# Optimization experiments

Hardware: AMD Instinct MI355X
Metric: run time of the kernel (lower is better)

Reference implementation:

```python
import jax, jax.numpy as jnp
import numpy as np

ALPHA = 100.0
EPS = 1e-12  # matches torch F.normalize default eps


def l2norm(v, axis):
    n = jnp.linalg.norm(v, axis=axis, keepdims=True)
    return v / jnp.maximum(n, EPS)


def setup_inputs() -> dict:
    key = jax.random.key(0)
    k1, k2 = jax.random.split(key)
    x = jax.random.normal(k1, (32, 128, 64, 64), dtype=jnp.float32)
    centroids = jax.random.uniform(k2, (64, 128), dtype=jnp.float32)
    return {"x": x, "centroids": centroids}


def reference(x, centroids):
    N, C, H, W = x.shape
    K = centroids.shape[0]
    # descriptor-wise L2 normalization over channel dim
    x = l2norm(x, axis=1)
    xf = x.reshape(N, C, H * W)  # [N, C, S]
    # 1x1 conv with weight = 2*alpha*centroids, bias = -alpha*||centroids||
    bias = -ALPHA * jnp.linalg.norm(centroids, axis=1)  # [K]
    logits = 2.0 * ALPHA * jnp.einsum('kc,ncs->nks', centroids, xf) + bias[None, :, None]
    a = jax.nn.softmax(logits, axis=1)  # soft assignment over clusters, [N, K, S]
    # vlad[n,k,c] = sum_s a[n,k,s] * (x[n,c,s] - centroids[k,c])
    #            = (a @ x^T)       - (sum_s a) * centroids   (GEMM form)
    vlad = jnp.einsum('nks,ncs->nkc', a, xf) - a.sum(axis=-1)[:, :, None] * centroids[None, :, :]
    vlad = l2norm(vlad, axis=2)            # intra-normalization
    vlad = vlad.reshape(N, K * C)
    vlad = l2norm(vlad, axis=1)            # final L2 normalization
    return vlad
```

## Files before the change

kernel.cpp:

```cpp
#include <hip/hip_runtime.h>
#include <math.h>

#define ALPHA_F 100.0f

constexpr int N_ = 32, C_ = 128, K_ = 64, S_ = 4096;
constexpr int NCHUNK = 8, SCHUNK = S_ / NCHUNK;
constexpr int ST = 128, NSUB = SCHUNK / ST;
constexpr int NT = 512;

typedef __attribute__((ext_vector_type(8))) short bf16x8;
typedef __attribute__((ext_vector_type(4))) float f32x4;

__device__ __forceinline__ short f2b(float f) {
  union { float f; unsigned u; } v; v.f = f;
  unsigned r = v.u + 0x7FFFu + ((v.u >> 16) & 1u);
  return (short)(r >> 16);
}
__device__ __forceinline__ float b2f(short b) {
  union { unsigned u; float f; } v; v.u = ((unsigned)(unsigned short)b) << 16;
  return v.f;
}
__device__ __forceinline__ unsigned pk2(short a, short b) {
  return ((unsigned)(unsigned short)a) | (((unsigned)(unsigned short)b) << 16);
}
#define BARRIER() do { asm volatile("s_waitcnt lgkmcnt(0)" ::: "memory"); \
                       __builtin_amdgcn_s_barrier(); } while (0)

__global__ __launch_bounds__(NT, 2)
void nv_stage1(const float* __restrict__ x, const float* __restrict__ cent,
               float* __restrict__ vlad_part, float* __restrict__ asum_part) {
  __shared__ short x2h[ST][136];
  __shared__ short x2l[ST][136];
  __shared__ short xbh[C_][136];
  __shared__ short cl_s[K_][136];
  __shared__ short a_th[K_][136];
  __shared__ float invn_s[ST];
  __shared__ float bias_s[K_];

  float* scratch = (float*)&a_th[0][0];

  const int t = threadIdx.x;
  const int l = t & 63, w = t >> 6;
  const int l16 = l & 15, g = l >> 4;
  const int cq = t >> 4, so = t & 15;
  const int chunk = blockIdx.x, n = blockIdx.y;
  const int sb = w * 16, cb = w * 16;

  const float* xg = x + (size_t)n * C_ * S_ + (size_t)chunk * SCHUNK;

  float xr[4][8];
  #pragma unroll
  for (int i = 0; i < 4; ++i) {
    const float* p = xg + (size_t)(cq * 4 + i) * S_ + so * 8;
    float4 u = *(const float4*)p, v = *(const float4*)(p + 4);
    xr[i][0] = u.x; xr[i][1] = u.y; xr[i][2] = u.z; xr[i][3] = u.w;
    xr[i][4] = v.x; xr[i][5] = v.y; xr[i][6] = v.z; xr[i][7] = v.w;
  }

  {
    const float* cr = cent + (t & 63) * C_ + w * 16;
    float ss = 0.f;
    #pragma unroll
    for (int h = 0; h < 4; ++h) {
      float4 v = *(const float4*)(cr + h * 4);
      ss += v.x * v.x + v.y * v.y + v.z * v.z + v.w * v.w;
    }
    scratch[w * 64 + (t & 63)] = ss;
  }
  {
    const int k = t >> 3, c0 = (t & 7) * 16;
    const float* cr = cent + k * C_ + c0;
    unsigned* dst = (unsigned*)&cl_s[k][c0];
    #pragma unroll
    for (int h = 0; h < 4; ++h) {
      float4 v = *(const float4*)(cr + h * 4);
      short a0 = f2b(v.x - b2f(f2b(v.x))), a1 = f2b(v.y - b2f(f2b(v.y)));
      short a2 = f2b(v.z - b2f(f2b(v.z))), a3 = f2b(v.w - b2f(f2b(v.w)));
      dst[h * 2 + 0] = pk2(a0, a1);
      dst[h * 2 + 1] = pk2(a2, a3);
    }
  }
  bf16x8 chf[4][4];
  #pragma unroll
  for (int nt2 = 0; nt2 < 4; ++nt2)
    #pragma unroll
    for (int ks = 0; ks < 4; ++ks) {
      const float* cr = cent + (nt2 * 16 + l16) * C_ + ks * 32 + g * 8;
      float4 a = *(const float4*)cr, b = *(const float4*)(cr + 4);
      bf16x8 f;
      f[0] = f2b(a.x); f[1] = f2b(a.y); f[2] = f2b(a.z); f[3] = f2b(a.w);
      f[4] = f2b(b.x); f[5] = f2b(b.y); f[6] = f2b(b.z); f[7] = f2b(b.w);
      chf[nt2][ks] = f;
    }
  __syncthreads();
  if (t < 64) {
    float ss = 0.f;
    #pragma unroll
    for (int q = 0; q < 8; ++q) ss += scratch[q * 64 + t];
    bias_s[t] = -ALPHA_F * sqrtf(ss);
  }
  __syncthreads();
  float bias_r[4];
  #pragma unroll
  for (int nt2 = 0; nt2 < 4; ++nt2) bias_r[nt2] = bias_s[nt2 * 16 + l16];

  f32x4 acc2[4];
  #pragma unroll
  for (int nt2 = 0; nt2 < 4; ++nt2) { f32x4 z = {0.f, 0.f, 0.f, 0.f}; acc2[nt2] = z; }
  float asum_acc[4] = {0.f, 0.f, 0.f, 0.f};

  for (int st = 0; st < NSUB; ++st) {
    BARRIER();
    float ss[8];
    #pragma unroll
    for (int j = 0; j < 8; ++j)
      ss[j] = xr[0][j] * xr[0][j] + xr[1][j] * xr[1][j]
            + xr[2][j] * xr[2][j] + xr[3][j] * xr[3][j];
    #pragma unroll
    for (int j = 0; j < 8; ++j) {
      ss[j] += __shfl_xor(ss[j], 16);
      ss[j] += __shfl_xor(ss[j], 32);
    }
    if (g == 0) {
      float4 w0 = make_float4(ss[0], ss[1], ss[2], ss[3]);
      float4 w1 = make_float4(ss[4], ss[5], ss[6], ss[7]);
      *(float4*)&scratch[w * 132 + so * 8]     = w0;
      *(float4*)&scratch[w * 132 + so * 8 + 4] = w1;
    }
    BARRIER();
    if (t < ST) {
      float s2 = 0.f;
      #pragma unroll
      for (int q = 0; q < 8; ++q) s2 += scratch[q * 132 + t];
      invn_s[t] = 1.0f / fmaxf(sqrtf(s2), 1e-12f);
    }
    BARRIER();
    {
      float4 i0 = *(float4*)&invn_s[so * 8], i1 = *(float4*)&invn_s[so * 8 + 4];
      float inj[8] = {i0.x, i0.y, i0.z, i0.w, i1.x, i1.y, i1.z, i1.w};
      #pragma unroll
      for (int i = 0; i < 4; ++i)
        #pragma unroll
        for (int j = 0; j < 8; ++j) xr[i][j] *= inj[j];
      #pragma unroll
      for (int i = 0; i < 4; ++i) {
        bf16x8 r;
        #pragma unroll
        for (int j = 0; j < 8; ++j) r[j] = f2b(xr[i][j]);
        *(bf16x8*)&xbh[cq * 4 + i][so * 8] = r;
      }
      #pragma unroll
      for (int j = 0; j < 8; ++j) {
        int s = so * 8 + j;
        int pc = (((cq >> 1) ^ (so & 7)) * 8) + (cq & 1) * 4;
        short h0 = f2b(xr[0][j]), h1 = f2b(xr[1][j]);
        short h2 = f2b(xr[2][j]), h3 = f2b(xr[3][j]);
        uint2 ph; ph.x = pk2(h0, h1); ph.y = pk2(h2, h3);
        *(uint2*)&x2h[s][pc] = ph;
        short e0 = f2b(xr[0][j] - b2f(h0)), e1 = f2b(xr[1][j] - b2f(h1));
        short e2 = f2b(xr[2][j] - b2f(h2)), e3 = f2b(xr[3][j] - b2f(h3));
        uint2 pl; pl.x = pk2(e0, e1); pl.y = pk2(e2, e3);
        *(uint2*)&x2l[s][pc] = pl;
      }
    }
    if (st + 1 < NSUB) {
      const float* pg = xg + (st + 1) * ST + so * 8;
      #pragma unroll
      for (int i = 0; i < 4; ++i) {
        const float* p = pg + (size_t)(cq * 4 + i) * S_;
        float4 u = *(const float4*)p, v = *(const float4*)(p + 4);
        xr[i][0] = u.x; xr[i][1] = u.y; xr[i][2] = u.z; xr[i][3] = u.w;
        xr[i][4] = v.x; xr[i][5] = v.y; xr[i][6] = v.z; xr[i][7] = v.w;
      }
    }
    BARRIER();
    bf16x8 ah[4], al[4];
    {
      int s = sb + l16;
      int nu = (s >> 3) & 7;
      #pragma unroll
      for (int ks = 0; ks < 4; ++ks) {
        int pc = ((ks * 4 + g) ^ nu) * 8;
        ah[ks] = *(const bf16x8*)&x2h[s][pc];
        al[ks] = *(const bf16x8*)&x2l[s][pc];
      }
    }
    f32x4 acc1[4];
    #pragma unroll
    for (int nt2 = 0; nt2 < 4; ++nt2) { f32x4 z = {0.f, 0.f, 0.f, 0.f}; acc1[nt2] = z; }
    #pragma unroll
    for (int nt2 = 0; nt2 < 4; ++nt2)
      #pragma unroll
      for (int ks = 0; ks < 4; ++ks) {
        acc1[nt2] = __builtin_amdgcn_mfma_f32_16x16x32_bf16(ah[ks], chf[nt2][ks], acc1[nt2], 0, 0, 0);
        acc1[nt2] = __builtin_amdgcn_mfma_f32_16x16x32_bf16(al[ks], chf[nt2][ks], acc1[nt2], 0, 0, 0);
        bf16x8 clf = *(const bf16x8*)&cl_s[nt2 * 16 + l16][ks * 32 + g * 8];
        acc1[nt2] = __builtin_amdgcn_mfma_f32_16x16x32_bf16(ah[ks], clf, acc1[nt2], 0, 0, 0);
      }
    {
      float v[4][4];
      #pragma unroll
      for (int nt2 = 0; nt2 < 4; ++nt2)
        #pragma unroll
        for (int i = 0; i < 4; ++i)
          v[nt2][i] = 2.f * ALPHA_F * acc1[nt2][i] + bias_r[nt2];
      float mx[4], sm[4];
      #pragma unroll
      for (int i = 0; i < 4; ++i) {
        mx[i] = fmaxf(fmaxf(v[0][i], v[1][i]), fmaxf(v[2][i], v[3][i]));
        mx[i] = fmaxf(mx[i], __shfl_xor(mx[i], 1));
        mx[i] = fmaxf(mx[i], __shfl_xor(mx[i], 2));
        mx[i] = fmaxf(mx[i], __shfl_xor(mx[i], 4));
        mx[i] = fmaxf(mx[i], __shfl_xor(mx[i], 8));
        sm[i] = 0.f;
      }
      #pragma unroll
      for (int nt2 = 0; nt2 < 4; ++nt2)
        #pragma unroll
        for (int i = 0; i < 4; ++i) {
          float e = __expf(v[nt2][i] - mx[i]);
          v[nt2][i] = e; sm[i] += e;
        }
      #pragma unroll
      for (int i = 0; i < 4; ++i) {
        sm[i] += __shfl_xor(sm[i], 1);
        sm[i] += __shfl_xor(sm[i], 2);
        sm[i] += __shfl_xor(sm[i], 4);
        sm[i] += __shfl_xor(sm[i], 8);
        sm[i] = 1.0f / sm[i];
      }
      #pragma unroll
      for (int nt2 = 0; nt2 < 4; ++nt2) {
        float a0 = v[nt2][0] * sm[0], a1 = v[nt2][1] * sm[1];
        float a2 = v[nt2][2] * sm[2], a3 = v[nt2][3] * sm[3];
        asum_acc[nt2] += a0 + a1 + a2 + a3;
        uint2 pa; pa.x = pk2(f2b(a0), f2b(a1)); pa.y = pk2(f2b(a2), f2b(a3));
        *(uint2*)&a_th[nt2 * 16 + l16][sb + g * 4] = pa;
      }
    }
    BARRIER();
    bf16x8 xq[4];
    #pragma unroll
    for (int ks = 0; ks < 4; ++ks)
      xq[ks] = *(const bf16x8*)&xbh[cb + l16][ks * 32 + g * 8];
    #pragma unroll
    for (int nt2 = 0; nt2 < 4; ++nt2)
      #pragma unroll
      for (int ks = 0; ks < 4; ++ks) {
        bf16x8 bq = *(const bf16x8*)&a_th[nt2 * 16 + l16][ks * 32 + g * 8];
        acc2[nt2] = __builtin_amdgcn_mfma_f32_16x16x32_bf16(xq[ks], bq, acc2[nt2], 0, 0, 0);
      }
  }

  BARRIER();
  #pragma unroll
  for (int nt2 = 0; nt2 < 4; ++nt2) {
    float vv = asum_acc[nt2];
    vv += __shfl_xor(vv, 16);
    vv += __shfl_xor(vv, 32);
    if (g == 0) scratch[2048 + w * 64 + nt2 * 16 + l16] = vv;
  }
  const size_t base = (size_t)(n * NCHUNK + chunk) * (K_ * C_);
  #pragma unroll
  for (int nt2 = 0; nt2 < 4; ++nt2) {
    int k = nt2 * 16 + l16;
    float4 o = make_float4(acc2[nt2][0], acc2[nt2][1], acc2[nt2][2], acc2[nt2][3]);
    *(float4*)&vlad_part[base + (size_t)k * C_ + cb + g * 4] = o;
  }
  BARRIER();
  if (t < 64) {
    float sum2 = 0.f;
    #pragma unroll
    for (int q = 0; q < 8; ++q) sum2 += scratch[2048 + q * 64 + t];
    asum_part[(n * NCHUNK + chunk) * K_ + t] = sum2;
  }
}

__global__ __launch_bounds__(256, 1)
void nv_stage2(const float* __restrict__ vlad_part, const float* __restrict__ asum_part,
               const float* __restrict__ cent, float* __restrict__ out) {
  __shared__ float asum_s[K_];
  __shared__ float redw[4];
  const int t = threadIdx.x, n = blockIdx.x;

  if (t < K_) {
    float s = 0.f;
    for (int ch = 0; ch < NCHUNK; ++ch) s += asum_part[(n * NCHUNK + ch) * K_ + t];
    asum_s[t] = s;
  }
  __syncthreads();

  float4 vp[8];
  float scl[8];
  float tot = 0.f;
  #pragma unroll
  for (int r = 0; r < 8; ++r) {
    const int f = t + 256 * r;
    const int k = f >> 5, c = (f & 31) * 4;
    float4 acc = make_float4(0.f, 0.f, 0.f, 0.f);
    for (int ch = 0; ch < NCHUNK; ++ch) {
      float4 v = *(const float4*)&vlad_part[((size_t)(n * NCHUNK + ch) * K_ + k) * C_ + c];
      acc.x += v.x; acc.y += v.y; acc.z += v.z; acc.w += v.w;
    }
    const float as = asum_s[k];
    float4 cw = *(const float4*)&cent[k * C_ + c];
    acc.x -= as * cw.x; acc.y -= as * cw.y; acc.z -= as * cw.z; acc.w -= as * cw.w;
    float ssq = acc.x * acc.x + acc.y * acc.y + acc.z * acc.z + acc.w * acc.w;
    #pragma unroll
    for (int wd = 1; wd <= 16; wd <<= 1) ssq += __shfl_xor(ssq, wd);
    float sc = 1.0f / fmaxf(sqrtf(ssq), 1e-12f);
    vp[r] = acc; scl[r] = sc;
    tot += ssq * sc * sc * (1.0f / 32.0f);
  }
  #pragma unroll
  for (int wd = 1; wd <= 32; wd <<= 1) tot += __shfl_xor(tot, wd);
  if ((t & 63) == 0) redw[t >> 6] = tot;
  __syncthreads();
  const float total = redw[0] + redw[1] + redw[2] + redw[3];
  const float rfin = 1.0f / fmaxf(sqrtf(total), 1e-12f);

  #pragma unroll
  for (int r = 0; r < 8; ++r) {
    const int f = t + 256 * r;
    const int k = f >> 5, c = (f & 31) * 4;
    const float s = scl[r] * rfin;
    float4 o = make_float4(vp[r].x * s, vp[r].y * s, vp[r].z * s, vp[r].w * s);
    *(float4*)&out[(size_t)n * (K_ * C_) + k * C_ + c] = o;
  }
}

extern "C" void kernel_launch(void* const* d_in, const int* in_sizes, int n_in,
                              void* d_out, int out_size, void* d_ws, size_t ws_size,
                              hipStream_t stream) {
  const float* x    = (const float*)d_in[0];
  const float* cent = (const float*)d_in[1];
  float* out = (float*)d_out;

  float* vlad_part = (float*)d_ws;
  float* asum_part = vlad_part + (size_t)N_ * NCHUNK * K_ * C_;

  dim3 g1(NCHUNK, N_);
  nv_stage1<<<g1, NT, 0, stream>>>(x, cent, vlad_part, asum_part);
  nv_stage2<<<N_, 256, 0, stream>>>(vlad_part, asum_part, cent, out);
}
```

Measured before the change: 46.47 us.

## Switch to fp16 split MFMA, defer normalization, double chunks, split stage2

Replaces the bf16 hi/lo split GEMMs with fp16 hi/lo split MFMAs. The first GEMM now runs on raw x loaded straight from global memory, and the per-column inverse norm is applied to the logits and assignments afterwards, so the normalized x2h/x2l LDS tiles are gone. LDS is packed into one byte buffer with swizzled centroid tiles. NCHUNK goes from 8 to 16 and the occupancy hint from 2 to 4 blocks per CU, for more parallelism. Stage 2 is split into a wider per-(n,k-block) kernel plus a small final-scaling kernel, which adds an extra launch and more global traffic. fp16 range and precision risks apply because raw x is unnormalized and x is now read from global memory twice.

After: 65.42 us. +40.8%, slower.

```diff
diff --git a/kernel.cpp b/kernel.cpp
--- a/kernel.cpp
+++ b/kernel.cpp
@@ -4,40 +4,37 @@
 #define ALPHA_F 100.0f
 
 constexpr int N_ = 32, C_ = 128, K_ = 64, S_ = 4096;
-constexpr int NCHUNK = 8, SCHUNK = S_ / NCHUNK;
+constexpr int NCHUNK = 16, SCHUNK = S_ / NCHUNK;
 constexpr int ST = 128, NSUB = SCHUNK / ST;
 constexpr int NT = 512;
 
-typedef __attribute__((ext_vector_type(8))) short bf16x8;
+typedef _Float16 f16;
+typedef __attribute__((ext_vector_type(4))) _Float16 f16x4;
+typedef __attribute__((ext_vector_type(8))) _Float16 f16x8;
 typedef __attribute__((ext_vector_type(4))) float f32x4;
 
-__device__ __forceinline__ short f2b(float f) {
-  union { float f; unsigned u; } v; v.f = f;
-  unsigned r = v.u + 0x7FFFu + ((v.u >> 16) & 1u);
-  return (short)(r >> 16);
-}
-__device__ __forceinline__ float b2f(short b) {
-  union { unsigned u; float f; } v; v.u = ((unsigned)(unsigned short)b) << 16;
-  return v.f;
-}
-__device__ __forceinline__ unsigned pk2(short a, short b) {
-  return ((unsigned)(unsigned short)a) | (((unsigned)(unsigned short)b) << 16);
-}
+constexpr int XBH = 0;
+constexpr int ASB = 34816;
+constexpr int CLS = 52224;
+constexpr int CHS = 68608;
+constexpr int INV = 80896;
+constexpr int BIA = 81408;
+constexpr int LDS_SZ = 81664;
+
 #define BARRIER() do { asm volatile("s_waitcnt lgkmcnt(0)" ::: "memory"); \
                        __builtin_amdgcn_s_barrier(); } while (0)
 
-__global__ __launch_bounds__(NT, 2)
+__global__ __launch_bounds__(NT, 4)
 void nv_stage1(const float* __restrict__ x, const float* __restrict__ cent,
                float* __restrict__ vlad_part, float* __restrict__ asum_part) {
-  __shared__ short x2h[ST][136];
-  __shared__ short x2l[ST][136];
-  __shared__ short xbh[C_][136];
-  __shared__ short cl_s[K_][136];
-  __shared__ short a_th[K_][136];
-  __shared__ float invn_s[ST];
-  __shared__ float bias_s[K_];
-
-  float* scratch = (float*)&a_th[0][0];
+  __shared__ __align__(16) unsigned char lds[LDS_SZ];
+  ushort* xbh  = (ushort*)(lds + XBH);
+  ushort* a_s  = (ushort*)(lds + ASB);
+  float*  scr  = (float*)(lds + ASB);
+  ushort* cls  = (ushort*)(lds + CLS);
+  ushort* chs  = (ushort*)(lds + CHS);
+  float*  invn = (float*)(lds + INV);
+  float*  bias_s = (float*)(lds + BIA);
 
   const int t = threadIdx.x;
   const int l = t & 63, w = t >> 6;
@@ -58,45 +55,49 @@
   }
 
   {
-    const float* cr = cent + (t & 63) * C_ + w * 16;
+    const float* cr = cent + l * C_ + w * 16;
     float ss = 0.f;
     #pragma unroll
     for (int h = 0; h < 4; ++h) {
       float4 v = *(const float4*)(cr + h * 4);
       ss += v.x * v.x + v.y * v.y + v.z * v.z + v.w * v.w;
     }
-    scratch[w * 64 + (t & 63)] = ss;
+    scr[w * 64 + l] = ss;
   }
   {
-    const int k = t >> 3, c0 = (t & 7) * 16;
-    const float* cr = cent + k * C_ + c0;
-    unsigned* dst = (unsigned*)&cl_s[k][c0];
-    #pragma unroll
-    for (int h = 0; h < 4; ++h) {
-      float4 v = *(const float4*)(cr + h * 4);
-      short a0 = f2b(v.x - b2f(f2b(v.x))), a1 = f2b(v.y - b2f(f2b(v.y)));
-      short a2 = f2b(v.z - b2f(f2b(v.z))), a3 = f2b(v.w - b2f(f2b(v.w)));
-      dst[h * 2 + 0] = pk2(a0, a1);
-      dst[h * 2 + 1] = pk2(a2, a3);
-    }
-  }
-  bf16x8 chf[4][4];
-  #pragma unroll
-  for (int nt2 = 0; nt2 < 4; ++nt2)
-    #pragma unroll
-    for (int ks = 0; ks < 4; ++ks) {
-      const float* cr = cent + (nt2 * 16 + l16) * C_ + ks * 32 + g * 8;
-      float4 a = *(const float4*)cr, b = *(const float4*)(cr + 4);
-      bf16x8 f;
-      f[0] = f2b(a.x); f[1] = f2b(a.y); f[2] = f2b(a.z); f[3] = f2b(a.w);
-      f[4] = f2b(b.x); f[5] = f2b(b.y); f[6] = f2b(b.z); f[7] = f2b(b.w);
-      chf[nt2][ks] = f;
-    }
+    const int k = t >> 3, c7 = t & 7;
+    const float* cr = cent + k * C_ + c7 * 16;
+    f16x8 lo0, lo1;
+    #pragma unroll
+    for (int h = 0; h < 8; ++h) {
+      float v0 = cr[h], v1 = cr[8 + h];
+      lo0[h] = (f16)(v0 - (float)((f16)v0));
+      lo1[h] = (f16)(v1 - (float)((f16)v1));
+    }
+    *(f16x8*)&cls[k * 128 + ((2 * c7) ^ (k & 15)) * 8]     = lo0;
+    *(f16x8*)&cls[k * 128 + ((2 * c7 + 1) ^ (k & 15)) * 8] = lo1;
+  }
+  if (t < 384) {
+    const int kl = t >> 3, c7 = t & 7;
+    const float* cr = cent + (16 + kl) * C_ + c7 * 16;
+    f16x8 h0v, h1v;
+    #pragma unroll
+    for (int h = 0; h < 8; ++h) { h0v[h] = (f16)cr[h]; h1v[h] = (f16)cr[8 + h]; }
+    *(f16x8*)&chs[kl * 128 + ((2 * c7) ^ (kl & 15)) * 8]     = h0v;
+    *(f16x8*)&chs[kl * 128 + ((2 * c7 + 1) ^ (kl & 15)) * 8] = h1v;
+  }
+  f16x8 chf0[4];
+  #pragma unroll
+  for (int ks = 0; ks < 4; ++ks) {
+    const float* cr = cent + l16 * C_ + ks * 32 + g * 8;
+    #pragma unroll
+    for (int h = 0; h < 8; ++h) chf0[ks][h] = (f16)cr[h];
+  }
   __syncthreads();
   if (t < 64) {
     float ss = 0.f;
     #pragma unroll
-    for (int q = 0; q < 8; ++q) ss += scratch[q * 64 + t];
+    for (int q = 0; q < 8; ++q) ss += scr[q * 64 + t];
     bias_s[t] = -ALPHA_F * sqrtf(ss);
   }
   __syncthreads();
@@ -106,105 +107,80 @@
 
   f32x4 acc2[4];
   #pragma unroll
-  for (int nt2 = 0; nt2 < 4; ++nt2) { f32x4 z = {0.f, 0.f, 0.f, 0.f}; acc2[nt2] = z; }
+  for (int nt2 = 0; nt2 < 4; ++nt2) { f32x4 z = {0.f,0.f,0.f,0.f}; acc2[nt2] = z; }
   float asum_acc[4] = {0.f, 0.f, 0.f, 0.f};
 
   for (int st = 0; st < NSUB; ++st) {
-    BARRIER();
-    float ss[8];
-    #pragma unroll
-    for (int j = 0; j < 8; ++j)
-      ss[j] = xr[0][j] * xr[0][j] + xr[1][j] * xr[1][j]
-            + xr[2][j] * xr[2][j] + xr[3][j] * xr[3][j];
-    #pragma unroll
-    for (int j = 0; j < 8; ++j) {
-      ss[j] += __shfl_xor(ss[j], 16);
-      ss[j] += __shfl_xor(ss[j], 32);
-    }
-    if (g == 0) {
-      float4 w0 = make_float4(ss[0], ss[1], ss[2], ss[3]);
-      float4 w1 = make_float4(ss[4], ss[5], ss[6], ss[7]);
-      *(float4*)&scratch[w * 132 + so * 8]     = w0;
-      *(float4*)&scratch[w * 132 + so * 8 + 4] = w1;
+    {
+      float ssj[8];
+      #pragma unroll
+      for (int j = 0; j < 8; ++j) {
+        ssj[j] = xr[0][j]*xr[0][j] + xr[1][j]*xr[1][j] + xr[2][j]*xr[2][j] + xr[3][j]*xr[3][j];
+        ssj[j] += __shfl_xor(ssj[j], 16);
+        ssj[j] += __shfl_xor(ssj[j], 32);
+      }
+      if (g == 0) {
+        *(float4*)&scr[w * 128 + so * 8]     = make_float4(ssj[0], ssj[1], ssj[2], ssj[3]);
+        *(float4*)&scr[w * 128 + so * 8 + 4] = make_float4(ssj[4], ssj[5], ssj[6], ssj[7]);
+      }
+      #pragma unroll
+      for (int i = 0; i < 4; ++i) {
+        f16x8 r;
+        #pragma unroll
+        for (int j = 0; j < 8; ++j) r[j] = (f16)xr[i][j];
+        *(f16x8*)&xbh[(cq * 4 + i) * 136 + so * 8] = r;
+      }
     }
     BARRIER();
     if (t < ST) {
       float s2 = 0.f;
       #pragma unroll
-      for (int q = 0; q < 8; ++q) s2 += scratch[q * 132 + t];
-      invn_s[t] = 1.0f / fmaxf(sqrtf(s2), 1e-12f);
+      for (int q = 0; q < 8; ++q) s2 += scr[q * 128 + t];
+      invn[t] = 1.0f / fmaxf(sqrtf(s2), 1e-12f);
     }
     BARRIER();
+
     {
-      float4 i0 = *(float4*)&invn_s[so * 8], i1 = *(float4*)&invn_s[so * 8 + 4];
-      float inj[8] = {i0.x, i0.y, i0.z, i0.w, i1.x, i1.y, i1.z, i1.w};
-      #pragma unroll
-      for (int i = 0; i < 4; ++i)
-        #pragma unroll
-        for (int j = 0; j < 8; ++j) xr[i][j] *= inj[j];
-      #pragma unroll
-      for (int i = 0; i < 4; ++i) {
-        bf16x8 r;
-        #pragma unroll
-        for (int j = 0; j < 8; ++j) r[j] = f2b(xr[i][j]);
-        *(bf16x8*)&xbh[cq * 4 + i][so * 8] = r;
-      }
-      #pragma unroll
-      for (int j = 0; j < 8; ++j) {
-        int s = so * 8 + j;
-        int pc = (((cq >> 1) ^ (so & 7)) * 8) + (cq & 1) * 4;
-        short h0 = f2b(xr[0][j]), h1 = f2b(xr[1][j]);
-        short h2 = f2b(xr[2][j]), h3 = f2b(xr[3][j]);
-        uint2 ph; ph.x = pk2(h0, h1); ph.y = pk2(h2, h3);
-        *(uint2*)&x2h[s][pc] = ph;
-        short e0 = f2b(xr[0][j] - b2f(h0)), e1 = f2b(xr[1][j] - b2f(h1));
-        short e2 = f2b(xr[2][j] - b2f(h2)), e3 = f2b(xr[3][j] - b2f(h3));
-        uint2 pl; pl.x = pk2(e0, e1); pl.y = pk2(e2, e3);
-        *(uint2*)&x2l[s][pc] = pl;
-      }
-    }
-    if (st + 1 < NSUB) {
-      const float* pg = xg + (st + 1) * ST + so * 8;
-      #pragma unroll
-      for (int i = 0; i < 4; ++i) {
-        const float* p = pg + (size_t)(cq * 4 + i) * S_;
-        float4 u = *(const float4*)p, v = *(const float4*)(p + 4);
-        xr[i][0] = u.x; xr[i][1] = u.y; xr[i][2] = u.z; xr[i][3] = u.w;
-        xr[i][4] = v.x; xr[i][5] = v.y; xr[i][6] = v.z; xr[i][7] = v.w;
-      }
-    }
-    BARRIER();
-    bf16x8 ah[4], al[4];
-    {
-      int s = sb + l16;
-      int nu = (s >> 3) & 7;
+      f32x4 acc1[4];
+      #pragma unroll
+      for (int nt2 = 0; nt2 < 4; ++nt2) { f32x4 z = {0.f,0.f,0.f,0.f}; acc1[nt2] = z; }
       #pragma unroll
       for (int ks = 0; ks < 4; ++ks) {
-        int pc = ((ks * 4 + g) ^ nu) * 8;
-        ah[ks] = *(const bf16x8*)&x2h[s][pc];
-        al[ks] = *(const bf16x8*)&x2l[s][pc];
-      }
-    }
-    f32x4 acc1[4];
-    #pragma unroll
-    for (int nt2 = 0; nt2 < 4; ++nt2) { f32x4 z = {0.f, 0.f, 0.f, 0.f}; acc1[nt2] = z; }
-    #pragma unroll
-    for (int nt2 = 0; nt2 < 4; ++nt2)
-      #pragma unroll
-      for (int ks = 0; ks < 4; ++ks) {
-        acc1[nt2] = __builtin_amdgcn_mfma_f32_16x16x32_bf16(ah[ks], chf[nt2][ks], acc1[nt2], 0, 0, 0);
-        acc1[nt2] = __builtin_amdgcn_mfma_f32_16x16x32_bf16(al[ks], chf[nt2][ks], acc1[nt2], 0, 0, 0);
-        bf16x8 clf = *(const bf16x8*)&cl_s[nt2 * 16 + l16][ks * 32 + g * 8];
-        acc1[nt2] = __builtin_amdgcn_mfma_f32_16x16x32_bf16(ah[ks], clf, acc1[nt2], 0, 0, 0);
-      }
-    {
-      float v[4][4];
+        float xa[8];
+        const float* pcol = xg + st * ST + sb + l16 + (size_t)(ks * 32 + g * 8) * S_;
+        #pragma unroll
+        for (int j = 0; j < 8; ++j) xa[j] = pcol[(size_t)j * S_];
+        f16x8 ah, al;
+        #pragma unroll
+        for (int j = 0; j < 8; ++j) {
+          f16 h = (f16)xa[j];
+          ah[j] = h;
+          al[j] = (f16)(xa[j] - (float)h);
+        }
+        f16x8 bh[4], bl[4];
+        bh[0] = chf0[ks];
+        #pragma unroll
+        for (int nt2 = 1; nt2 < 4; ++nt2)
+          bh[nt2] = *(const f16x8*)&chs[((nt2 - 1) * 16 + l16) * 128 + (((ks * 4 + g) ^ l16) * 8)];
+        #pragma unroll
+        for (int nt2 = 0; nt2 < 4; ++nt2)
+          bl[nt2] = *(const f16x8*)&cls[(nt2 * 16 + l16) * 128 + (((ks * 4 + g) ^ l16) * 8)];
+        #pragma unroll
+        for (int nt2 = 0; nt2 < 4; ++nt2) {
+          acc1[nt2] = __builtin_amdgcn_mfma_f32_16x16x32_f16(ah, bh[nt2], acc1[nt2], 0, 0, 0);
+          acc1[nt2] = __builtin_amdgcn_mfma_f32_16x16x32_f16(ah, bl[nt2], acc1[nt2], 0, 0, 0);
+          acc1[nt2] = __builtin_amdgcn_mfma_f32_16x16x32_f16(al, bh[nt2], acc1[nt2], 0, 0, 0);
+        }
+      }
+      float inv4[4];
+      #pragma unroll
+      for (int i = 0; i < 4; ++i) inv4[i] = invn[sb + 4 * g + i];
+      float v[4][4], mx[4], sm[4];
       #pragma unroll
       for (int nt2 = 0; nt2 < 4; ++nt2)
         #pragma unroll
         for (int i = 0; i < 4; ++i)
-          v[nt2][i] = 2.f * ALPHA_F * acc1[nt2][i] + bias_r[nt2];
-      float mx[4], sm[4];
+          v[nt2][i] = 2.f * ALPHA_F * acc1[nt2][i] * inv4[i] + bias_r[nt2];
       #pragma unroll
       for (int i = 0; i < 4; ++i) {
         mx[i] = fmaxf(fmaxf(v[0][i], v[1][i]), fmaxf(v[2][i], v[3][i]));
@@ -217,16 +193,11 @@
       #pragma unroll
       for (int nt2 = 0; nt2 < 4; ++nt2)
         #pragma unroll
-        for (int i = 0; i < 4; ++i) {
-          float e = __expf(v[nt2][i] - mx[i]);
-          v[nt2][i] = e; sm[i] += e;
-        }
+        for (int i = 0; i < 4; ++i) { float e = __expf(v[nt2][i] - mx[i]); v[nt2][i] = e; sm[i] += e; }
       #pragma unroll
       for (int i = 0; i < 4; ++i) {
-        sm[i] += __shfl_xor(sm[i], 1);
-        sm[i] += __shfl_xor(sm[i], 2);
-        sm[i] += __shfl_xor(sm[i], 4);
-        sm[i] += __shfl_xor(sm[i], 8);
+        sm[i] += __shfl_xor(sm[i], 1); sm[i] += __shfl_xor(sm[i], 2);
+        sm[i] += __shfl_xor(sm[i], 4); sm[i] += __shfl_xor(sm[i], 8);
         sm[i] = 1.0f / sm[i];
       }
       #pragma unroll
@@ -234,98 +205,96 @@
         float a0 = v[nt2][0] * sm[0], a1 = v[nt2][1] * sm[1];
         float a2 = v[nt2][2] * sm[2], a3 = v[nt2][3] * sm[3];
         asum_acc[nt2] += a0 + a1 + a2 + a3;
-        uint2 pa; pa.x = pk2(f2b(a0), f2b(a1)); pa.y = pk2(f2b(a2), f2b(a3));
-        *(uint2*)&a_th[nt2 * 16 + l16][sb + g * 4] = pa;
+        f16x4 av;
+        av[0] = (f16)(a0 * inv4[0]); av[1] = (f16)(a1 * inv4[1]);
+        av[2] = (f16)(a2 * inv4[2]); av[3] = (f16)(a3 * inv4[3]);
+        *(f16x4*)&a_s[(nt2 * 16 + l16) * 136 + sb + g * 4] = av;
       }
     }
     BARRIER();
-    bf16x8 xq[4];
-    #pragma unroll
-    for (int ks = 0; ks < 4; ++ks)
-      xq[ks] = *(const bf16x8*)&xbh[cb + l16][ks * 32 + g * 8];
-    #pragma unroll
-    for (int nt2 = 0; nt2 < 4; ++nt2)
-      #pragma unroll
-      for (int ks = 0; ks < 4; ++ks) {
-        bf16x8 bq = *(const bf16x8*)&a_th[nt2 * 16 + l16][ks * 32 + g * 8];
-        acc2[nt2] = __builtin_amdgcn_mfma_f32_16x16x32_bf16(xq[ks], bq, acc2[nt2], 0, 0, 0);
-      }
-  }
-
-  BARRIER();
+
+    if (st + 1 < NSUB) {
+      const float* pg = xg + (st + 1) * ST + so * 8;
+      #pragma unroll
+      for (int i = 0; i < 4; ++i) {
+        const float* p = pg + (size_t)(cq * 4 + i) * S_;
+        float4 u = *(const float4*)p, vq = *(const float4*)(p + 4);
+        xr[i][0] = u.x; xr[i][1] = u.y; xr[i][2] = u.z; xr[i][3] = u.w;
+        xr[i][4] = vq.x; xr[i][5] = vq.y; xr[i][6] = vq.z; xr[i][7] = vq.w;
+      }
+    }
+    #pragma unroll
+    for (int ks = 0; ks < 4; ++ks) {
+      f16x8 xq = *(const f16x8*)&xbh[(cb + l16) * 136 + ks * 32 + g * 8];
+      #pragma unroll
+      for (int nt2 = 0; nt2 < 4; ++nt2) {
+        f16x8 pa = *(const f16x8*)&a_s[(nt2 * 16 + l16) * 136 + ks * 32 + g * 8];
+        acc2[nt2] = __builtin_amdgcn_mfma_f32_16x16x32_f16(xq, pa, acc2[nt2], 0, 0, 0);
+      }
+    }
+    BARRIER();
+  }
+
   #pragma unroll
   for (int nt2 = 0; nt2 < 4; ++nt2) {
     float vv = asum_acc[nt2];
-    vv += __shfl_xor(vv, 16);
-    vv += __shfl_xor(vv, 32);
-    if (g == 0) scratch[2048 + w * 64 + nt2 * 16 + l16] = vv;
+    vv += __shfl_xor(vv, 16); vv += __shfl_xor(vv, 32);
+    if (g == 0) scr[w * 64 + nt2 * 16 + l16] = vv;
   }
   const size_t base = (size_t)(n * NCHUNK + chunk) * (K_ * C_);
   #pragma unroll
   for (int nt2 = 0; nt2 < 4; ++nt2) {
-    int k = nt2 * 16 + l16;
     float4 o = make_float4(acc2[nt2][0], acc2[nt2][1], acc2[nt2][2], acc2[nt2][3]);
-    *(float4*)&vlad_part[base + (size_t)k * C_ + cb + g * 4] = o;
+    *(float4*)&vlad_part[base + (size_t)(nt2 * 16 + l16) * C_ + cb + g * 4] = o;
   }
   BARRIER();
   if (t < 64) {
-    float sum2 = 0.f;
-    #pragma unroll
-    for (int q = 0; q < 8; ++q) sum2 += scratch[2048 + q * 64 + t];
-    asum_part[(n * NCHUNK + chunk) * K_ + t] = sum2;
+    float s2 = 0.f;
+    #pragma unroll
+    for (int q = 0; q < 8; ++q) s2 += scr[q * 64 + t];
+    asum_part[(n * NCHUNK + chunk) * K_ + t] = s2;
   }
 }
 
-__global__ __launch_bounds__(256, 1)
-void nv_stage2(const float* __restrict__ vlad_part, const float* __restrict__ asum_part,
-               const float* __restrict__ cent, float* __restrict__ out) {
-  __shared__ float asum_s[K_];
-  __shared__ float redw[4];
+__global__ __launch_bounds__(256)
+void nv_stage2a(const float* __restrict__ vlad_part, const float* __restrict__ asum_part,
+                const float* __restrict__ cent, float* __restrict__ vlad_n,
+                float* __restrict__ rssq) {
+  const int t = threadIdx.x, b = blockIdx.x;
+  const int n = b >> 3, k8 = (b & 7) * 8;
+  const int kl = t >> 5, c4 = (t & 31) * 4;
+  const int k = k8 + kl;
+  float as = 0.f;
+  for (int ch = 0; ch < NCHUNK; ++ch) as += asum_part[(n * NCHUNK + ch) * K_ + k];
+  float4 acc = make_float4(0.f, 0.f, 0.f, 0.f);
+  for (int ch = 0; ch < NCHUNK; ++ch) {
+    float4 v = *(const float4*)&vlad_part[((size_t)(n * NCHUNK + ch) * K_ + k) * C_ + c4];
+    acc.x += v.x; acc.y += v.y; acc.z += v.z; acc.w += v.w;
+  }
+  float4 cw = *(const float4*)&cent[k * C_ + c4];
+  acc.x -= as * cw.x; acc.y -= as * cw.y; acc.z -= as * cw.z; acc.w -= as * cw.w;
+  float ssq = acc.x * acc.x + acc.y * acc.y + acc.z * acc.z + acc.w * acc.w;
+  #pragma unroll
+  for (int m = 1; m <= 16; m <<= 1) ssq += __shfl_xor(ssq, m);
+  float scl = 1.0f / fmaxf(sqrtf(ssq), 1e-12f);
+  *(float4*)&vlad_n[(size_t)n * (K_ * C_) + k * C_ + c4] =
+      make_float4(acc.x * scl, acc.y * scl, acc.z * scl, acc.w * scl);
+  if ((t & 31) == 0) rssq[n * K_ + k] = ssq * scl * scl;
+}
+
+__global__ __launch_bounds__(256)
+void nv_stage2b(const float* __restrict__ vlad_n, const float* __restrict__ rssq,
+                float* __restrict__ out) {
   const int t = threadIdx.x, n = blockIdx.x;
-
-  if (t < K_) {
-    float s = 0.f;
-    for (int ch = 0; ch < NCHUNK; ++ch) s += asum_part[(n * NCHUNK + ch) * K_ + t];
-    asum_s[t] = s;
-  }
-  __syncthreads();
-
-  float4 vp[8];
-  float scl[8];
   float tot = 0.f;
+  for (int k2 = 0; k2 < K_; ++k2) tot += rssq[n * K_ + k2];
+  const float rfin = 1.0f / fmaxf(sqrtf(tot), 1e-12f);
   #pragma unroll
   for (int r = 0; r < 8; ++r) {
-    const int f = t + 256 * r;
-    const int k = f >> 5, c = (f & 31) * 4;
-    float4 acc = make_float4(0.f, 0.f, 0.f, 0.f);
-    for (int ch = 0; ch < NCHUNK; ++ch) {
-      float4 v = *(const float4*)&vlad_part[((size_t)(n * NCHUNK + ch) * K_ + k) * C_ + c];
-      acc.x += v.x; acc.y += v.y; acc.z += v.z; acc.w += v.w;
-    }
-    const float as = asum_s[k];
-    float4 cw = *(const float4*)&cent[k * C_ + c];
-    acc.x -= as * cw.x; acc.y -= as * cw.y; acc.z -= as * cw.z; acc.w -= as * cw.w;
-    float ssq = acc.x * acc.x + acc.y * acc.y + acc.z * acc.z + acc.w * acc.w;
-    #pragma unroll
-    for (int wd = 1; wd <= 16; wd <<= 1) ssq += __shfl_xor(ssq, wd);
-    float sc = 1.0f / fmaxf(sqrtf(ssq), 1e-12f);
-    vp[r] = acc; scl[r] = sc;
-    tot += ssq * sc * sc * (1.0f / 32.0f);
-  }
-  #pragma unroll
-  for (int wd = 1; wd <= 32; wd <<= 1) tot += __shfl_xor(tot, wd);
-  if ((t & 63) == 0) redw[t >> 6] = tot;
-  __syncthreads();
-  const float total = redw[0] + redw[1] + redw[2] + redw[3];
-  const float rfin = 1.0f / fmaxf(sqrtf(total), 1e-12f);
-
-  #pragma unroll
-  for (int r = 0; r < 8; ++r) {
-    const int f = t + 256 * r;
-    const int k = f >> 5, c = (f & 31) * 4;
-    const float s = scl[r] * rfin;
-    float4 o = make_float4(vp[r].x * s, vp[r].y * s, vp[r].z * s, vp[r].w * s);
-    *(float4*)&out[(size_t)n * (K_ * C_) + k * C_ + c] = o;
+    int idx = t * 4 + r * 1024;
+    float4 v = *(const float4*)&vlad_n[(size_t)n * (K_ * C_) + idx];
+    *(float4*)&out[(size_t)n * (K_ * C_) + idx] =
+        make_float4(v.x * rfin, v.y * rfin, v.z * rfin, v.w * rfin);
   }
 }
 
@@ -338,8 +307,11 @@
 
   float* vlad_part = (float*)d_ws;
   float* asum_part = vlad_part + (size_t)N_ * NCHUNK * K_ * C_;
+  float* vlad_n    = asum_part + (size_t)N_ * NCHUNK * K_;
+  float* rssq      = vlad_n + (size_t)N_ * K_ * C_;
 
   dim3 g1(NCHUNK, N_);
   nv_stage1<<<g1, NT, 0, stream>>>(x, cent, vlad_part, asum_part);
-  nv_stage2<<<N_, 256, 0, stream>>>(vlad_part, asum_part, cent, out);
+  nv_stage2a<<<N_ * 8, 256, 0, stream>>>(vlad_part, asum_part, cent, vlad_n, rssq);
+  nv_stage2b<<<N_, 256, 0, stream>>>(vlad_n, rssq, out);
 }
```
